# Performance work log

Hardware: AMD Instinct MI355X
Metric: run time of the kernel (lower is better)

The kernel has to match this reference:

```python
import jax, jax.numpy as jnp
import numpy as np

B, S, HID = 1, 2048, 4096
NH, NKV, HD = 32, 8, 128
GROUPS = NH // NKV
EPS = 1e-8
THETA = 10000.0
SCALE = HD ** -0.5
INIT = 0.02


def setup_inputs() -> dict:
    key = jax.random.key(0)
    ks = jax.random.split(key, 8)
    return {
        "hidden_states": jax.random.normal(ks[0], (B, S, HID), jnp.float32),
        "position_ids": jnp.arange(S, dtype=jnp.int32)[None, :],
        "wq": jax.random.normal(ks[1], (HID, NH * HD), jnp.float32) * INIT,
        "wk": jax.random.normal(ks[2], (HID, NKV * HD), jnp.float32) * INIT,
        "wv": jax.random.normal(ks[3], (HID, NKV * HD), jnp.float32) * INIT,
        "wo": jax.random.normal(ks[4], (NH * HD, HID), jnp.float32) * INIT,
        "memory": jax.random.normal(ks[5], (NKV, HD, HD), jnp.float32) * INIT,
        "norm_m": jax.random.uniform(ks[6], (NKV, HD, HD), jnp.float32) * 0.5 + 0.5,
        "beta": jnp.zeros((1,), jnp.float32),
    }


def _rotate_half(x):
    h = x.shape[-1] // 2
    return jnp.concatenate([-x[..., h:], x[..., :h]], axis=-1)


def _rope(position_ids):
    inv_freq = 1.0 / (THETA ** (jnp.arange(0, HD, 2, dtype=jnp.float32) / HD))  # [HD/2]
    freqs = position_ids.astype(jnp.float32)[:, :, None] * inv_freq[None, None, :]  # [B,S,HD/2]
    emb = jnp.concatenate([freqs, freqs], axis=-1)  # [B,S,HD]
    return jnp.cos(emb)[:, None], jnp.sin(emb)[:, None]  # [B,1,S,HD] each


def reference(hidden_states, position_ids, wq, wk, wv, wo, memory, norm_m, beta):
    # projections -> [B, heads, S, HD]
    q = (hidden_states @ wq).reshape(B, S, NH, HD).transpose(0, 2, 1, 3)
    k = (hidden_states @ wk).reshape(B, S, NKV, HD).transpose(0, 2, 1, 3)
    v = (hidden_states @ wv).reshape(B, S, NKV, HD).transpose(0, 2, 1, 3)

    # ---- retrieve from compressive memory (pre-RoPE Q, as in original) ----
    qf = jax.nn.elu(q) + 1.0
    qn = qf / (qf.sum(axis=-1, keepdims=True) + EPS)            # [B,NH,S,HD]
    mem_t = jnp.tile(memory[None], (1, GROUPS, 1, 1))            # torch .repeat == tile: head h -> memory[h % NKV]
    norm_t = jnp.tile(jnp.swapaxes(norm_m, -1, -2)[None], (1, GROUPS, 1, 1))
    mem_out = jnp.matmul(qn, mem_t) / (jnp.matmul(qn, norm_t) + EPS)  # [B,NH,S,HD]

    # ---- delta-rule memory update (no-grad side effect in torch) ----
    kf = jax.nn.elu(k) + 1.0
    kn = kf / (kf.sum(axis=-1, keepdims=True) + EPS)             # [B,NKV,S,HD]
    v_ret = jnp.matmul(kn, memory) / (jnp.matmul(kn, jnp.swapaxes(norm_m, -1, -2)) + EPS)
    delta = jnp.einsum('bhsd,bhse->hde', kn, v - v_ret)          # sum over batch
    updated_memory = memory + delta
    updated_norm = norm_m + kn.sum(axis=2, keepdims=True)[0]     # [NKV,1,HD] broadcast

    # ---- RoPE ----
    cos, sin = _rope(position_ids)
    q = q * cos + _rotate_half(q) * sin
    k = k * cos + _rotate_half(k) * sin

    # ---- causal attention with GQA (repeat_interleave for K/V) ----
    kr = jnp.repeat(k, GROUPS, axis=1)
    vr = jnp.repeat(v, GROUPS, axis=1)
    scores = jnp.einsum('bhqd,bhkd->bhqk', q, kr) * SCALE        # [B,NH,S,S]
    causal = jnp.tril(jnp.ones((S, S), dtype=bool))
    scores = jnp.where(causal, scores, jnp.finfo(scores.dtype).min)
    attn = jax.nn.softmax(scores, axis=-1)
    attn_out = jnp.einsum('bhqk,bhkd->bhqd', attn, vr)           # [B,NH,S,HD]

    # ---- sigmoid-gated combine + output projection ----
    gate = jax.nn.sigmoid(beta)                                   # [1]
    combined = gate * mem_out + (1.0 - gate) * attn_out
    out = combined.transpose(0, 2, 1, 3).reshape(B, S, NH * HD) @ wo
    return out, updated_memory, updated_norm
```

## Files before the change

### kernel.cpp

```cpp
#include <hip/hip_runtime.h>

#define S_LEN 2048
#define HID_DIM 4096
#define NH 32
#define NKV 8
#define HD 128
#define QKV_N 6144
#define SCALE_F 0.08838834764831845f

typedef unsigned short u16;
typedef __attribute__((ext_vector_type(8))) __bf16 bf16x8;
typedef __attribute__((ext_vector_type(4))) float f32x4;

__device__ __forceinline__ u16 f2bf(float f) {
  unsigned u = __float_as_uint(f);
  return (u16)((u + 0x7fffu + ((u >> 16) & 1u)) >> 16);
}
__device__ __forceinline__ float bf2f(u16 v) {
  return __uint_as_float((unsigned)v << 16);
}

__device__ __forceinline__ void gl_lds16(const u16* g, u16* l) {
  __builtin_amdgcn_global_load_lds(
      (const __attribute__((address_space(1))) unsigned int*)g,
      (__attribute__((address_space(3))) unsigned int*)l, 16, 0, 0);
}


__global__ void k_f32_to_bf16(const float* __restrict__ in, u16* __restrict__ out, long n4) {
  long i = (long)blockIdx.x * blockDim.x + threadIdx.x;
  if (i >= n4) return;
  float4 v = ((const float4*)in)[i];
  ushort4 o;
  o.x = f2bf(v.x); o.y = f2bf(v.y); o.z = f2bf(v.z); o.w = f2bf(v.w);
  ((ushort4*)out)[i] = o;
}

__global__ void k_tr64(const float* __restrict__ in, u16* __restrict__ out,
                       int ld_in, int ld_out, long in_bs, long out_bs) {
  __shared__ float tile[64][65];
  const float* A = in + (long)blockIdx.z * in_bs;
  u16* O = out + (long)blockIdx.z * out_bs;
  int r0 = blockIdx.y * 64, c0 = blockIdx.x * 64;
  int tx = threadIdx.x & 31, ty = threadIdx.x >> 5;
#pragma unroll
  for (int i = 0; i < 8; i++) {
    int r = ty + 8 * i;
    float2 v = *(const float2*)&A[(long)(r0 + r) * ld_in + c0 + 2 * tx];
    tile[r][2 * tx] = v.x;
    tile[r][2 * tx + 1] = v.y;
  }
  __syncthreads();
#pragma unroll
  for (int i = 0; i < 8; i++) {
    int c = ty + 8 * i;
    ushort2 o;
    o.x = f2bf(tile[2 * tx][c]);
    o.y = f2bf(tile[2 * tx + 1][c]);
    *(ushort2*)&O[(long)(c0 + c) * ld_out + r0 + 2 * tx] = o;
  }
}

__global__ void k_norm_to_bc(const float* __restrict__ norm, u16* __restrict__ bc) {
  int h = blockIdx.y;
  int i = blockIdx.x * 256 + threadIdx.x;
  bc[(long)h * 32768 + 16384 + i] = f2bf(norm[(long)h * 16384 + i]);
}


__global__ __launch_bounds__(512, 2) void k_gemm8(
    const u16* __restrict__ A, const u16* __restrict__ Bt, void* __restrict__ Cv,
    int kloop, int lda, int ldb, int ldc,
    long strideA, long strideB, long strideC, int bmodB, int obf) {
  __shared__ __align__(16) u16 lds[65536];
  const int bz = blockIdx.z;
  const u16* Ap = A + (long)bz * strideA;
  const u16* Bp = Bt + (long)(bz % bmodB) * strideB;
  const long coff = (long)bz * strideC;

  const int gx = gridDim.x, gy = gridDim.y;
  const int nwg = gx * gy;
  int id = blockIdx.y * gx + blockIdx.x;
  if (!(nwg & 7)) { int q = nwg >> 3; id = (id & 7) * q + (id >> 3); }
  const int m0 = (id % gy) * 256;
  const int n0 = (id / gy) * 256;

  const int tid = threadIdx.x, wid = tid >> 6, lane = tid & 63;
  const int l15 = lane & 15, lhi = lane >> 4;
  const int wm = wid >> 2, wn = wid & 3;

  const int srow = (wid << 3) + (lane >> 3);
  const int ssw = ((lane & 7) ^ (lane >> 3)) * 8;
  auto stA = [&](int d, int g, long kt) {
    gl_lds16(Ap + (long)(m0 + g * 64 + srow) * lda + kt + ssw,
             &lds[d * 32768 + (g * 64 + (wid << 3)) * 64]);
  };
  auto stB = [&](int d, int g, long kt) {
    gl_lds16(Bp + (long)(n0 + g * 64 + srow) * ldb + kt + ssw,
             &lds[d * 32768 + 16384 + (g * 64 + (wid << 3)) * 64]);
  };

  const int swb = l15 & 7;
  const int aBase = (wm * 128 + l15) * 64;
  const int bBase = 16384 + (wn * 64 + l15) * 64;
  const int ko0 = (lhi ^ swb) * 8;
  const int ko1 = ((4 + lhi) ^ swb) * 8;

  const int KT = kloop >> 6;
  const int NIT = KT >> 1;

  f32x4 acc[8][4];
#pragma unroll
  for (int i = 0; i < 8; i++)
#pragma unroll
    for (int j = 0; j < 4; j++) acc[i][j] = (f32x4){0.f, 0.f, 0.f, 0.f};

#pragma unroll
  for (int g = 0; g < 4; g++) stA(0, g, 0);
#pragma unroll
  for (int g = 0; g < 4; g++) stB(0, g, 0);
#pragma unroll
  for (int g = 0; g < 4; g++) stB(1, g, 64);
  asm volatile("s_waitcnt vmcnt(4)" ::: "memory");
  __builtin_amdgcn_s_barrier();
  asm volatile("" ::: "memory");

  for (int t = 0; t < NIT; ++t) {
    const long kA = (long)(2 * t + 1) * 64;
    const long kB0 = (long)(2 * t + 2) * 64;
    const long kB1 = (long)(2 * t + 3) * 64;
    const bool st0 = (2 * t + 2) < KT;
    const bool st1 = (2 * t + 3) < KT;
    const bool last = (t + 1 == NIT);

    {
      const u16* lb = &lds[0];
      bf16x8 Bf[4][2];
#pragma unroll
      for (int p = 0; p < 4; p++) {
        if (p == 0) {
#pragma unroll
          for (int ni = 0; ni < 4; ni++) {
            Bf[ni][0] = *(const bf16x8*)&lb[bBase + ni * 1024 + ko0];
            Bf[ni][1] = *(const bf16x8*)&lb[bBase + ni * 1024 + ko1];
          }
        }
        bf16x8 a0k0 = *(const bf16x8*)&lb[aBase + (2 * p) * 1024 + ko0];
        bf16x8 a0k1 = *(const bf16x8*)&lb[aBase + (2 * p) * 1024 + ko1];
        bf16x8 a1k0 = *(const bf16x8*)&lb[aBase + (2 * p + 1) * 1024 + ko0];
        bf16x8 a1k1 = *(const bf16x8*)&lb[aBase + (2 * p + 1) * 1024 + ko1];
        if (p == 0) { stA(1, 0, kA); stA(1, 1, kA); }
        else if (p == 1) { stA(1, 2, kA); stA(1, 3, kA); }
        else if (p == 2) { if (st0) { stB(0, 0, kB0); stB(0, 1, kB0); } }
        else { if (st0) { stB(0, 2, kB0); stB(0, 3, kB0); } }
        asm volatile("" ::: "memory");
        if (p == 3) {
          if (last) asm volatile("s_waitcnt vmcnt(0)" ::: "memory");
          else      asm volatile("s_waitcnt vmcnt(4)" ::: "memory");
        }
        __builtin_amdgcn_s_barrier();
        asm volatile("" ::: "memory");
        __builtin_amdgcn_s_setprio(1);
#pragma unroll
        for (int ni = 0; ni < 4; ni++) {
          acc[2 * p][ni] = __builtin_amdgcn_mfma_f32_16x16x32_bf16(a0k0, Bf[ni][0], acc[2 * p][ni], 0, 0, 0);
          acc[2 * p][ni] = __builtin_amdgcn_mfma_f32_16x16x32_bf16(a0k1, Bf[ni][1], acc[2 * p][ni], 0, 0, 0);
          acc[2 * p + 1][ni] = __builtin_amdgcn_mfma_f32_16x16x32_bf16(a1k0, Bf[ni][0], acc[2 * p + 1][ni], 0, 0, 0);
          acc[2 * p + 1][ni] = __builtin_amdgcn_mfma_f32_16x16x32_bf16(a1k1, Bf[ni][1], acc[2 * p + 1][ni], 0, 0, 0);
        }
        __builtin_amdgcn_s_setprio(0);
        asm volatile("" ::: "memory");
        __builtin_amdgcn_s_barrier();
        asm volatile("" ::: "memory");
      }
    }
    {
      const u16* lb = &lds[32768];
      bf16x8 Bf[4][2];
#pragma unroll
      for (int p = 0; p < 4; p++) {
        if (p == 0) {
#pragma unroll
          for (int ni = 0; ni < 4; ni++) {
            Bf[ni][0] = *(const bf16x8*)&lb[bBase + ni * 1024 + ko0];
            Bf[ni][1] = *(const bf16x8*)&lb[bBase + ni * 1024 + ko1];
          }
        }
        bf16x8 a0k0 = *(const bf16x8*)&lb[aBase + (2 * p) * 1024 + ko0];
        bf16x8 a0k1 = *(const bf16x8*)&lb[aBase + (2 * p) * 1024 + ko1];
        bf16x8 a1k0 = *(const bf16x8*)&lb[aBase + (2 * p + 1) * 1024 + ko0];
        bf16x8 a1k1 = *(const bf16x8*)&lb[aBase + (2 * p + 1) * 1024 + ko1];
        if (p == 0) { if (st0) { stA(0, 0, kB0); stA(0, 1, kB0); } }
        else if (p == 1) { if (st0) { stA(0, 2, kB0); stA(0, 3, kB0); } }
        else if (p == 2) { if (st1) { stB(1, 0, kB1); stB(1, 1, kB1); } }
        else { if (st1) { stB(1, 2, kB1); stB(1, 3, kB1); } }
        asm volatile("" ::: "memory");
        if (p == 3 && !last) asm volatile("s_waitcnt vmcnt(4)" ::: "memory");
        __builtin_amdgcn_s_barrier();
        asm volatile("" ::: "memory");
        __builtin_amdgcn_s_setprio(1);
#pragma unroll
        for (int ni = 0; ni < 4; ni++) {
          acc[2 * p][ni] = __builtin_amdgcn_mfma_f32_16x16x32_bf16(a0k0, Bf[ni][0], acc[2 * p][ni], 0, 0, 0);
          acc[2 * p][ni] = __builtin_amdgcn_mfma_f32_16x16x32_bf16(a0k1, Bf[ni][1], acc[2 * p][ni], 0, 0, 0);
          acc[2 * p + 1][ni] = __builtin_amdgcn_mfma_f32_16x16x32_bf16(a1k0, Bf[ni][0], acc[2 * p + 1][ni], 0, 0, 0);
          acc[2 * p + 1][ni] = __builtin_amdgcn_mfma_f32_16x16x32_bf16(a1k1, Bf[ni][1], acc[2 * p + 1][ni], 0, 0, 0);
        }
        __builtin_amdgcn_s_setprio(0);
        asm volatile("" ::: "memory");
        __builtin_amdgcn_s_barrier();
        asm volatile("" ::: "memory");
      }
    }
  }

#pragma unroll
  for (int mi = 0; mi < 8; mi++)
#pragma unroll
    for (int ni = 0; ni < 4; ni++)
#pragma unroll
      for (int j = 0; j < 4; j++) {
        long row = m0 + wm * 128 + mi * 16 + lhi * 4 + j;
        long col = n0 + wn * 64 + ni * 16 + l15;
        if (obf)
          ((u16*)Cv)[coff + row * ldc + col] = f2bf(acc[mi][ni][j]);
        else
          ((float*)Cv)[coff + row * ldc + col] = acc[mi][ni][j];
      }
}


__global__ void k_addp(const u16* __restrict__ p0, const u16* __restrict__ p1,
                       float* __restrict__ out) {
  long i = ((long)blockIdx.x * 256 + threadIdx.x) * 8;
  ushort4 a0 = *(const ushort4*)&p0[i], a1 = *(const ushort4*)&p0[i + 4];
  ushort4 b0 = *(const ushort4*)&p1[i], b1 = *(const ushort4*)&p1[i + 4];
  float4 o0, o1;
  o0.x = bf2f(a0.x) + bf2f(b0.x); o0.y = bf2f(a0.y) + bf2f(b0.y);
  o0.z = bf2f(a0.z) + bf2f(b0.z); o0.w = bf2f(a0.w) + bf2f(b0.w);
  o1.x = bf2f(a1.x) + bf2f(b1.x); o1.y = bf2f(a1.y) + bf2f(b1.y);
  o1.z = bf2f(a1.z) + bf2f(b1.z); o1.w = bf2f(a1.w) + bf2f(b1.w);
  *(float4*)&out[i] = o0;
  *(float4*)&out[i + 4] = o1;
}


__global__ void k_qnrope(const float* __restrict__ qkv, const int* __restrict__ pos,
                         u16* __restrict__ qnb, u16* __restrict__ qrb,
                         u16* __restrict__ knb, u16* __restrict__ krb,
                         float* __restrict__ knf) {
  int s = blockIdx.x, y = blockIdx.y, l = threadIdx.x;
  bool isq = y < NH;
  int h = isq ? y : y - NH;
  const float* row = qkv + (long)s * QKV_N + (isq ? h * HD : HID_DIM + h * HD);
  float x0 = row[l], x1 = row[l + 64];
  float f0 = x0 > 0.f ? x0 + 1.f : __expf(x0);
  float f1 = x1 > 0.f ? x1 + 1.f : __expf(x1);
  float sum = f0 + f1;
#pragma unroll
  for (int m = 32; m >= 1; m >>= 1) sum += __shfl_xor(sum, m);
  float inv = 1.f / (sum + 1e-8f);
  float y0 = f0 * inv, y1 = f1 * inv;
  long o = ((long)h * S_LEN + s) * HD;
  float p = (float)pos[s];
  float ang = p * expf(-(float)l * (9.210340371976184f / 64.0f));
  float c = cosf(ang), sn = sinf(ang);
  u16 r0 = f2bf(x0 * c - x1 * sn), r1 = f2bf(x1 * c + x0 * sn);
  if (isq) {
    qnb[o + l] = f2bf(y0); qnb[o + l + 64] = f2bf(y1);
    qrb[o + l] = r0; qrb[o + l + 64] = r1;
  } else {
    knb[o + l] = f2bf(y0); knb[o + l + 64] = f2bf(y1);
    knf[o + l] = y0; knf[o + l + 64] = y1;
    krb[o + l] = r0; krb[o + l + 64] = r1;
  }
}


__global__ void k_uvret(const u16* __restrict__ rawk, const float* __restrict__ qkv,
                        float* __restrict__ U) {
  int s = blockIdx.x, h = blockIdx.y, e = threadIdx.x;
  long base = ((long)h * S_LEN + s) * 256;
  float num = bf2f(rawk[base + e]), den = bf2f(rawk[base + 128 + e]);
  U[((long)h * S_LEN + s) * HD + e] =
      qkv[(long)s * QKV_N + HID_DIM + NKV * HD + h * HD + e] - num / (den + 1e-8f);
}


__global__ __launch_bounds__(256, 2) void k_flash3(
    const u16* __restrict__ qr, const u16* __restrict__ kr,
    const u16* __restrict__ vt, float* __restrict__ attn) {
  __shared__ u16 KV[2][16384];
  __shared__ u16 Ps[4][16 * 64];
  const int bx = blockIdx.x, h = blockIdx.y;
  const int hk = h >> 2;
  const int tid = threadIdx.x, wid = tid >> 6, lane = tid & 63;
  const int l15 = lane & 15, lhi = lane >> 4;
  const u16* qbase = qr + (long)h * S_LEN * HD;
  const u16* kb0 = kr + (long)hk * S_LEN * HD;
  const u16* vb0 = vt + (long)hk * HD * S_LEN;
  float* ob = attn + (long)h * S_LEN * HD;
  u16* P = Ps[wid];

  int kr_r[4], kr_sc[4], vr_r[4], vr_sc[4];
#pragma unroll
  for (int it = 0; it < 4; it++) {
    int chunk = it * 4 + wid;
    kr_r[it] = chunk * 4 + (lane >> 4);
    kr_sc[it] = ((lane & 15) * 8) ^ ((kr_r[it] & 7) * 8);
    vr_r[it] = chunk * 8 + (lane >> 3);
    vr_sc[it] = ((lane & 7) * 8) ^ ((vr_r[it] & 7) * 8);
  }

  for (int si = 0; si < 2; si++) {
    const int s = si ? (31 - bx) : bx;
    const int qs = s * 64 + wid * 16;
    bf16x8 aq[4];
#pragma unroll
    for (int kc = 0; kc < 4; kc++)
      aq[kc] = *(const bf16x8*)&qbase[(long)(qs + l15) * HD + kc * 32 + lhi * 8];
    f32x4 accO[8];
#pragma unroll
    for (int i = 0; i < 8; i++) accO[i] = (f32x4){0.f, 0.f, 0.f, 0.f};
    float rs[4] = {0.f, 0.f, 0.f, 0.f};

    if (si) __syncthreads();
    {
      u16* Kb = KV[0];
#pragma unroll
      for (int it = 0; it < 4; it++)
        gl_lds16(kb0 + (long)kr_r[it] * HD + kr_sc[it], &Kb[(it * 4 + wid) * 512]);
#pragma unroll
      for (int it = 0; it < 4; it++)
        gl_lds16(vb0 + (long)vr_r[it] * S_LEN + vr_sc[it], &Kb[8192 + (it * 4 + wid) * 512]);
    }
    int cur = 0;

    for (int t = 0; t <= s; t++) {
      asm volatile("s_waitcnt vmcnt(0)" ::: "memory");
      __syncthreads();
      if (t < s) {
        u16* Kb = KV[cur ^ 1];
        const long kt = (long)(t + 1) * 64;
#pragma unroll
        for (int it = 0; it < 4; it++)
          gl_lds16(kb0 + (kt + kr_r[it]) * HD + kr_sc[it], &Kb[(it * 4 + wid) * 512]);
#pragma unroll
        for (int it = 0; it < 4; it++)
          gl_lds16(vb0 + (long)vr_r[it] * S_LEN + kt + vr_sc[it], &Kb[8192 + (it * 4 + wid) * 512]);
      }
      const u16* Ks = KV[cur];
      const u16* Vs = Ks + 8192;

      f32x4 accS[4];
#pragma unroll
      for (int i = 0; i < 4; i++) accS[i] = (f32x4){0.f, 0.f, 0.f, 0.f};
#pragma unroll
      for (int ni = 0; ni < 4; ni++) {
        int row = ni * 16 + l15;
#pragma unroll
        for (int kc = 0; kc < 4; kc++) {
          bf16x8 bk = *(const bf16x8*)&Ks[row * 128 + ((kc * 32 + lhi * 8) ^ ((row & 7) * 8))];
          accS[ni] = __builtin_amdgcn_mfma_f32_16x16x32_bf16(aq[kc], bk, accS[ni], 0, 0, 0);
        }
      }
      const bool diag = (t == s);
#pragma unroll
      for (int ni = 0; ni < 4; ni++) {
        int col = t * 64 + ni * 16 + l15;
#pragma unroll
        for (int j = 0; j < 4; j++) {
          int row = qs + lhi * 4 + j;
          float p = (!diag || col <= row) ? __expf(accS[ni][j] * SCALE_F) : 0.f;
          rs[j] += p;
          int pr = lhi * 4 + j;
          P[pr * 64 + ((ni * 16 + l15) ^ ((pr & 7) * 8))] = f2bf(p);
        }
      }
      asm volatile("s_waitcnt lgkmcnt(0)" ::: "memory");
      __builtin_amdgcn_sched_barrier(0);
      bf16x8 ap[2];
#pragma unroll
      for (int ks = 0; ks < 2; ks++)
        ap[ks] = *(const bf16x8*)&P[l15 * 64 + ((ks * 32 + lhi * 8) ^ ((l15 & 7) * 8))];
#pragma unroll
      for (int nj = 0; nj < 8; nj++) {
        int row = nj * 16 + l15;
#pragma unroll
        for (int ks = 0; ks < 2; ks++) {
          bf16x8 bv = *(const bf16x8*)&Vs[row * 64 + ((ks * 32 + lhi * 8) ^ ((row & 7) * 8))];
          accO[nj] = __builtin_amdgcn_mfma_f32_16x16x32_bf16(ap[ks], bv, accO[nj], 0, 0, 0);
        }
      }
      cur ^= 1;
    }
#pragma unroll
    for (int j = 0; j < 4; j++) {
      float v = rs[j];
      v += __shfl_xor(v, 1);
      v += __shfl_xor(v, 2);
      v += __shfl_xor(v, 4);
      v += __shfl_xor(v, 8);
      rs[j] = 1.f / v;
    }
#pragma unroll
    for (int nj = 0; nj < 8; nj++)
#pragma unroll
      for (int j = 0; j < 4; j++)
        ob[(long)(qs + lhi * 4 + j) * HD + nj * 16 + l15] = accO[nj][j] * rs[j];
  }
}


__global__ void k_combine(const u16* __restrict__ rawq, const float* __restrict__ attn,
                          const float* __restrict__ beta, u16* __restrict__ comb) {
  int s = blockIdx.x, h = blockIdx.y, d = threadIdx.x;
  float g = 1.f / (1.f + __expf(-beta[0]));
  long b = ((long)h * S_LEN + s) * 256;
  float mo = bf2f(rawq[b + d]) / (bf2f(rawq[b + 128 + d]) + 1e-8f);
  float ao = attn[((long)h * S_LEN + s) * HD + d];
  comb[(long)s * HID_DIM + h * HD + d] = f2bf(g * mo + (1.f - g) * ao);
}


__global__ void k_delta_part(const float* __restrict__ knf, const float* __restrict__ U,
                             float* __restrict__ dpart) {
  int d0 = blockIdx.x * 16, h = blockIdx.y, c = blockIdx.z, e = threadIdx.x;
  const float* kh = knf + (long)h * S_LEN * HD + (long)c * 512 * HD;
  const float* Uh = U + (long)h * S_LEN * HD + (long)c * 512 * HD;
  float a[16];
#pragma unroll
  for (int d = 0; d < 16; d++) a[d] = 0.f;
  for (int s = 0; s < 512; s++) {
    float u = Uh[(long)s * HD + e];
    const float* kr = &kh[(long)s * HD + d0];
#pragma unroll
    for (int d = 0; d < 16; d++) a[d] += kr[d] * u;
  }
  long ob = (long)c * (NKV * HD * HD) + (long)h * HD * HD + (long)d0 * HD + e;
#pragma unroll
  for (int d = 0; d < 16; d++) dpart[ob + (long)d * HD] = a[d];
}

__global__ void k_delta_reduce(const float* __restrict__ dpart, const float* __restrict__ mem,
                               float* __restrict__ outmem) {
  long i = (long)blockIdx.x * 256 + threadIdx.x;
  const long N = (long)NKV * HD * HD;
  float a = dpart[i] + dpart[N + i] + dpart[2 * N + i] + dpart[3 * N + i];
  outmem[i] = mem[i] + a;
}

__global__ void k_norm_part(const float* __restrict__ knf, float* __restrict__ npart) {
  int c = blockIdx.x, h = blockIdx.y, j = threadIdx.x;
  const float* kh = knf + (long)h * S_LEN * HD + (long)c * 128 * HD;
  float a = 0.f;
  for (int s = 0; s < 128; s++) a += kh[(long)s * HD + j];
  npart[((long)c * NKV + h) * HD + j] = a;
}

__global__ void k_norm_write(const float* __restrict__ npart, const float* __restrict__ norm,
                             float* __restrict__ outn) {
  int h = blockIdx.x, j = threadIdx.x & 127;
  int r = blockIdx.y * 2 + (threadIdx.x >> 7);
  float cs = 0.f;
#pragma unroll
  for (int c = 0; c < 16; c++) cs += npart[((long)c * NKV + h) * HD + j];
  long o = (long)h * HD * HD + (long)r * HD + j;
  outn[o] = norm[o] + cs;
}


extern "C" void kernel_launch(void* const* d_in, const int* in_sizes, int n_in,
                              void* d_out, int out_size, void* d_ws, size_t ws_size,
                              hipStream_t stream) {
  const float* hs = (const float*)d_in[0];
  const int* pos = (const int*)d_in[1];
  const float* wq = (const float*)d_in[2];
  const float* wk = (const float*)d_in[3];
  const float* wv = (const float*)d_in[4];
  const float* wo = (const float*)d_in[5];
  const float* memf = (const float*)d_in[6];
  const float* normf = (const float*)d_in[7];
  const float* beta = (const float*)d_in[8];
  (void)in_sizes; (void)n_in; (void)out_size; (void)ws_size;

  float* out = (float*)d_out;
  float* out_mem = out + (long)S_LEN * HID_DIM;
  float* out_norm = out_mem + NKV * HD * HD;

  const size_t MB = 1u << 20;
  char* w = (char*)d_ws;
  u16* hsb    = (u16*)(w + 0);
  u16* qnb    = (u16*)(w + 0);
  u16* comb   = (u16*)(w + 0);
  float* dpart= (float*)(w + 0);
  float* npart= (float*)(w + 2 * MB);
  u16* wT6    = (u16*)(w + 16 * MB);
  u16* rawq   = (u16*)(w + 16 * MB);
  u16* woT    = (u16*)(w + 16 * MB);
  u16* rawk   = (u16*)(w + 48 * MB);
  u16* bc     = (u16*)(w + 57 * MB);
  u16* vtb    = (u16*)(w + 57 * MB + 512 * 1024);
  float* qkvf = (float*)(w + 66 * MB + 512 * 1024);
  float* attn = (float*)(w + 66 * MB + 512 * 1024);
  u16* p0     = (u16*)(w + 98 * MB + 512 * 1024);
  float* Ub   = (float*)(w + 114 * MB + 512 * 1024);
  float* knf  = (float*)(w + 122 * MB + 512 * 1024);
  u16* qrb    = (u16*)(w + 130 * MB + 512 * 1024);
  u16* p1     = (u16*)(w + 130 * MB + 512 * 1024);
  u16* krb    = (u16*)(w + 146 * MB + 512 * 1024);
  u16* knb    = (u16*)(w + 150 * MB + 512 * 1024);

  k_f32_to_bf16<<<dim3((S_LEN * HID_DIM / 4 + 255) / 256), dim3(256), 0, stream>>>(
      hs, hsb, (long)(S_LEN * HID_DIM / 4));
  k_tr64<<<dim3(64, 64, 1), dim3(256), 0, stream>>>(
      wq, wT6, HID_DIM, HID_DIM, 0L, 0L);
  k_tr64<<<dim3(16, 64, 1), dim3(256), 0, stream>>>(
      wk, wT6 + (long)HID_DIM * HID_DIM, 1024, HID_DIM, 0L, 0L);
  k_tr64<<<dim3(16, 64, 1), dim3(256), 0, stream>>>(
      wv, wT6 + (long)(HID_DIM + 1024) * HID_DIM, 1024, HID_DIM, 0L, 0L);
  k_gemm8<<<dim3(QKV_N / 256, S_LEN / 256, 1), dim3(512), 0, stream>>>(
      hsb, wT6, qkvf, HID_DIM, HID_DIM, HID_DIM, QKV_N, 0L, 0L, 0L, 1, 0);

  k_qnrope<<<dim3(S_LEN, NH + NKV), dim3(64), 0, stream>>>(
      qkvf, pos, qnb, qrb, knb, krb, knf);

  k_tr64<<<dim3(2, 32, NKV), dim3(256), 0, stream>>>(
      qkvf + HID_DIM + NKV * HD, vtb, QKV_N, S_LEN, 128L, (long)(HD * S_LEN));
  k_tr64<<<dim3(2, 2, NKV), dim3(256), 0, stream>>>(
      memf, bc, HD, HD, (long)(HD * HD), (long)(256 * HD));
  k_norm_to_bc<<<dim3(64, NKV), dim3(256), 0, stream>>>(normf, bc);

  k_gemm8<<<dim3(1, 8, NH), dim3(512), 0, stream>>>(
      qnb, bc, rawq, HD, HD, HD, 256, (long)(S_LEN * HD), (long)(256 * HD),
      (long)(S_LEN * 256), NKV, 1);
  k_gemm8<<<dim3(1, 8, NKV), dim3(512), 0, stream>>>(
      knb, bc, rawk, HD, HD, HD, 256, (long)(S_LEN * HD), (long)(256 * HD),
      (long)(S_LEN * 256), NKV, 1);

  k_uvret<<<dim3(S_LEN, NKV), dim3(128), 0, stream>>>(rawk, qkvf, Ub);

  k_flash3<<<dim3(16, NH), dim3(256), 0, stream>>>(qrb, krb, vtb, attn);

  k_combine<<<dim3(S_LEN, NH), dim3(128), 0, stream>>>(rawq, attn, beta, comb);

  k_tr64<<<dim3(64, 64, 1), dim3(256), 0, stream>>>(
      wo, woT, HID_DIM, HID_DIM, 0L, 0L);
  k_gemm8<<<dim3(HID_DIM / 256, S_LEN / 256, 2), dim3(512), 0, stream>>>(
      comb, woT, p0, 2048, HID_DIM, HID_DIM, HID_DIM,
      2048L, 2048L, (long)(p1 - p0), 2, 1);
  k_addp<<<dim3(S_LEN * HID_DIM / 2048), dim3(256), 0, stream>>>(p0, p1, out);

  k_delta_part<<<dim3(8, NKV, 4), dim3(128), 0, stream>>>(knf, Ub, dpart);
  k_delta_reduce<<<dim3(512), dim3(256), 0, stream>>>(dpart, memf, out_mem);
  k_norm_part<<<dim3(16, NKV), dim3(128), 0, stream>>>(knf, npart);
  k_norm_write<<<dim3(NKV, 64), dim3(256), 0, stream>>>(npart, normf, out_norm);
}
```

Baseline: 435.1 us.

## Fuse gated combine into flash epilogue and fold small memory-path kernels

The gated combine now happens in the flash-attention epilogue, which writes bf16 `comb` directly instead of a full fp32 attention buffer that a separate pass reread. The v - v_ret computation moves from its own kernel into the delta accumulation. The Q and K memory-retrieval GEMMs run as one batched launch through a new second A pointer. The fp32 copy of normalized K is dropped and the delta and norm reductions read the bf16 values. The aim is to cut memory traffic and launch count, at the cost of slightly lower precision in the memory-update outputs and extra rawq reads inside the attention kernel's epilogue.

```diff
diff --git a/kernel.cpp b/kernel.cpp
--- a/kernel.cpp
+++ b/kernel.cpp
@@ -69,12 +69,14 @@
 
 
 __global__ __launch_bounds__(512, 2) void k_gemm8(
-    const u16* __restrict__ A, const u16* __restrict__ Bt, void* __restrict__ Cv,
+    const u16* __restrict__ A, const u16* __restrict__ A2, int zsplit,
+    const u16* __restrict__ Bt, void* __restrict__ Cv,
     int kloop, int lda, int ldb, int ldc,
     long strideA, long strideB, long strideC, int bmodB, int obf) {
   __shared__ __align__(16) u16 lds[65536];
   const int bz = blockIdx.z;
-  const u16* Ap = A + (long)bz * strideA;
+  const u16* Ap = (bz < zsplit) ? (A + (long)bz * strideA)
+                                : (A2 + (long)(bz - zsplit) * strideA);
   const u16* Bp = Bt + (long)(bz % bmodB) * strideB;
   const long coff = (long)bz * strideC;
 
@@ -247,8 +249,7 @@
 
 __global__ void k_qnrope(const float* __restrict__ qkv, const int* __restrict__ pos,
                          u16* __restrict__ qnb, u16* __restrict__ qrb,
-                         u16* __restrict__ knb, u16* __restrict__ krb,
-                         float* __restrict__ knf) {
+                         u16* __restrict__ knb, u16* __restrict__ krb) {
   int s = blockIdx.x, y = blockIdx.y, l = threadIdx.x;
   bool isq = y < NH;
   int h = isq ? y : y - NH;
@@ -271,25 +272,15 @@
     qrb[o + l] = r0; qrb[o + l + 64] = r1;
   } else {
     knb[o + l] = f2bf(y0); knb[o + l + 64] = f2bf(y1);
-    knf[o + l] = y0; knf[o + l + 64] = y1;
     krb[o + l] = r0; krb[o + l + 64] = r1;
   }
 }
 
 
-__global__ void k_uvret(const u16* __restrict__ rawk, const float* __restrict__ qkv,
-                        float* __restrict__ U) {
-  int s = blockIdx.x, h = blockIdx.y, e = threadIdx.x;
-  long base = ((long)h * S_LEN + s) * 256;
-  float num = bf2f(rawk[base + e]), den = bf2f(rawk[base + 128 + e]);
-  U[((long)h * S_LEN + s) * HD + e] =
-      qkv[(long)s * QKV_N + HID_DIM + NKV * HD + h * HD + e] - num / (den + 1e-8f);
-}
-
-
-__global__ __launch_bounds__(256, 2) void k_flash3(
+__global__ __launch_bounds__(256, 2) void k_flash4(
     const u16* __restrict__ qr, const u16* __restrict__ kr,
-    const u16* __restrict__ vt, float* __restrict__ attn) {
+    const u16* __restrict__ vt, const u16* __restrict__ rawq,
+    const float* __restrict__ beta, u16* __restrict__ comb) {
   __shared__ u16 KV[2][16384];
   __shared__ u16 Ps[4][16 * 64];
   const int bx = blockIdx.x, h = blockIdx.y;
@@ -299,8 +290,8 @@
   const u16* qbase = qr + (long)h * S_LEN * HD;
   const u16* kb0 = kr + (long)hk * S_LEN * HD;
   const u16* vb0 = vt + (long)hk * HD * S_LEN;
-  float* ob = attn + (long)h * S_LEN * HD;
   u16* P = Ps[wid];
+  const float g = 1.f / (1.f + __expf(-beta[0]));
 
   int kr_r[4], kr_sc[4], vr_r[4], vr_sc[4];
 #pragma unroll
@@ -406,36 +397,34 @@
 #pragma unroll
     for (int nj = 0; nj < 8; nj++)
 #pragma unroll
-      for (int j = 0; j < 4; j++)
-        ob[(long)(qs + lhi * 4 + j) * HD + nj * 16 + l15] = accO[nj][j] * rs[j];
-  }
-}
-
-
-__global__ void k_combine(const u16* __restrict__ rawq, const float* __restrict__ attn,
-                          const float* __restrict__ beta, u16* __restrict__ comb) {
-  int s = blockIdx.x, h = blockIdx.y, d = threadIdx.x;
-  float g = 1.f / (1.f + __expf(-beta[0]));
-  long b = ((long)h * S_LEN + s) * 256;
-  float mo = bf2f(rawq[b + d]) / (bf2f(rawq[b + 128 + d]) + 1e-8f);
-  float ao = attn[((long)h * S_LEN + s) * HD + d];
-  comb[(long)s * HID_DIM + h * HD + d] = f2bf(g * mo + (1.f - g) * ao);
-}
-
-
-__global__ void k_delta_part(const float* __restrict__ knf, const float* __restrict__ U,
-                             float* __restrict__ dpart) {
+      for (int j = 0; j < 4; j++) {
+        int row = qs + lhi * 4 + j;
+        int col = nj * 16 + l15;
+        long rb = ((long)h * S_LEN + row) * 256 + col;
+        float mo = bf2f(rawq[rb]) / (bf2f(rawq[rb + 128]) + 1e-8f);
+        float ao = accO[nj][j] * rs[j];
+        comb[(long)row * HID_DIM + h * HD + col] = f2bf(g * mo + (1.f - g) * ao);
+      }
+  }
+}
+
+
+__global__ void k_delta_part(const u16* __restrict__ knb, const u16* __restrict__ rawk,
+                             const float* __restrict__ qkv, float* __restrict__ dpart) {
   int d0 = blockIdx.x * 16, h = blockIdx.y, c = blockIdx.z, e = threadIdx.x;
-  const float* kh = knf + (long)h * S_LEN * HD + (long)c * 512 * HD;
-  const float* Uh = U + (long)h * S_LEN * HD + (long)c * 512 * HD;
+  const u16* kh = knb + (long)h * S_LEN * HD + (long)c * 512 * HD;
+  const u16* rk = rawk + ((long)h * S_LEN + (long)c * 512) * 256;
+  const float* vb = qkv + HID_DIM + NKV * HD + h * HD + (long)c * 512 * QKV_N;
   float a[16];
 #pragma unroll
   for (int d = 0; d < 16; d++) a[d] = 0.f;
   for (int s = 0; s < 512; s++) {
-    float u = Uh[(long)s * HD + e];
-    const float* kr = &kh[(long)s * HD + d0];
-#pragma unroll
-    for (int d = 0; d < 16; d++) a[d] += kr[d] * u;
+    float num = bf2f(rk[(long)s * 256 + e]);
+    float den = bf2f(rk[(long)s * 256 + 128 + e]);
+    float u = vb[(long)s * QKV_N + e] - num / (den + 1e-8f);
+    const u16* kr = &kh[(long)s * HD + d0];
+#pragma unroll
+    for (int d = 0; d < 16; d++) a[d] += bf2f(kr[d]) * u;
   }
   long ob = (long)c * (NKV * HD * HD) + (long)h * HD * HD + (long)d0 * HD + e;
 #pragma unroll
@@ -450,11 +439,11 @@
   outmem[i] = mem[i] + a;
 }
 
-__global__ void k_norm_part(const float* __restrict__ knf, float* __restrict__ npart) {
+__global__ void k_norm_part(const u16* __restrict__ knb, float* __restrict__ npart) {
   int c = blockIdx.x, h = blockIdx.y, j = threadIdx.x;
-  const float* kh = knf + (long)h * S_LEN * HD + (long)c * 128 * HD;
+  const u16* kh = knb + (long)h * S_LEN * HD + (long)c * 128 * HD;
   float a = 0.f;
-  for (int s = 0; s < 128; s++) a += kh[(long)s * HD + j];
+  for (int s = 0; s < 128; s++) a += bf2f(kh[(long)s * HD + j]);
   npart[((long)c * NKV + h) * HD + j] = a;
 }
 
@@ -493,8 +482,6 @@
   u16* hsb    = (u16*)(w + 0);
   u16* qnb    = (u16*)(w + 0);
   u16* comb   = (u16*)(w + 0);
-  float* dpart= (float*)(w + 0);
-  float* npart= (float*)(w + 2 * MB);
   u16* wT6    = (u16*)(w + 16 * MB);
   u16* rawq   = (u16*)(w + 16 * MB);
   u16* woT    = (u16*)(w + 16 * MB);
@@ -502,13 +489,12 @@
   u16* bc     = (u16*)(w + 57 * MB);
   u16* vtb    = (u16*)(w + 57 * MB + 512 * 1024);
   float* qkvf = (float*)(w + 66 * MB + 512 * 1024);
-  float* attn = (float*)(w + 66 * MB + 512 * 1024);
   u16* p0     = (u16*)(w + 98 * MB + 512 * 1024);
-  float* Ub   = (float*)(w + 114 * MB + 512 * 1024);
-  float* knf  = (float*)(w + 122 * MB + 512 * 1024);
   u16* qrb    = (u16*)(w + 130 * MB + 512 * 1024);
   u16* p1     = (u16*)(w + 130 * MB + 512 * 1024);
   u16* krb    = (u16*)(w + 146 * MB + 512 * 1024);
+  float* dpart= (float*)(w + 146 * MB + 512 * 1024);
+  float* npart= (float*)(w + 148 * MB + 512 * 1024);
   u16* knb    = (u16*)(w + 150 * MB + 512 * 1024);
 
   k_f32_to_bf16<<<dim3((S_LEN * HID_DIM / 4 + 255) / 256), dim3(256), 0, stream>>>(
@@ -520,10 +506,11 @@
   k_tr64<<<dim3(16, 64, 1), dim3(256), 0, stream>>>(
       wv, wT6 + (long)(HID_DIM + 1024) * HID_DIM, 1024, HID_DIM, 0L, 0L);
   k_gemm8<<<dim3(QKV_N / 256, S_LEN / 256, 1), dim3(512), 0, stream>>>(
-      hsb, wT6, qkvf, HID_DIM, HID_DIM, HID_DIM, QKV_N, 0L, 0L, 0L, 1, 0);
+      hsb, hsb, 1 << 30, wT6, qkvf, HID_DIM, HID_DIM, HID_DIM, QKV_N,
+      0L, 0L, 0L, 1, 0);
 
   k_qnrope<<<dim3(S_LEN, NH + NKV), dim3(64), 0, stream>>>(
-      qkvf, pos, qnb, qrb, knb, krb, knf);
+      qkvf, pos, qnb, qrb, knb, krb);
 
   k_tr64<<<dim3(2, 32, NKV), dim3(256), 0, stream>>>(
       qkvf + HID_DIM + NKV * HD, vtb, QKV_N, S_LEN, 128L, (long)(HD * S_LEN));
@@ -531,28 +518,21 @@
       memf, bc, HD, HD, (long)(HD * HD), (long)(256 * HD));
   k_norm_to_bc<<<dim3(64, NKV), dim3(256), 0, stream>>>(normf, bc);
 
-  k_gemm8<<<dim3(1, 8, NH), dim3(512), 0, stream>>>(
-      qnb, bc, rawq, HD, HD, HD, 256, (long)(S_LEN * HD), (long)(256 * HD),
-      (long)(S_LEN * 256), NKV, 1);
-  k_gemm8<<<dim3(1, 8, NKV), dim3(512), 0, stream>>>(
-      knb, bc, rawk, HD, HD, HD, 256, (long)(S_LEN * HD), (long)(256 * HD),
-      (long)(S_LEN * 256), NKV, 1);
-
-  k_uvret<<<dim3(S_LEN, NKV), dim3(128), 0, stream>>>(rawk, qkvf, Ub);
-
-  k_flash3<<<dim3(16, NH), dim3(256), 0, stream>>>(qrb, krb, vtb, attn);
-
-  k_combine<<<dim3(S_LEN, NH), dim3(128), 0, stream>>>(rawq, attn, beta, comb);
+  k_gemm8<<<dim3(1, 8, NH + NKV), dim3(512), 0, stream>>>(
+      qnb, knb, NH, bc, rawq, HD, HD, HD, 256,
+      (long)(S_LEN * HD), (long)(256 * HD), (long)(S_LEN * 256), NKV, 1);
+
+  k_flash4<<<dim3(16, NH), dim3(256), 0, stream>>>(qrb, krb, vtb, rawq, beta, comb);
+
+  k_delta_part<<<dim3(8, NKV, 4), dim3(128), 0, stream>>>(knb, rawk, qkvf, dpart);
+  k_delta_reduce<<<dim3(512), dim3(256), 0, stream>>>(dpart, memf, out_mem);
+  k_norm_part<<<dim3(16, NKV), dim3(128), 0, stream>>>(knb, npart);
+  k_norm_write<<<dim3(NKV, 64), dim3(256), 0, stream>>>(npart, normf, out_norm);
 
   k_tr64<<<dim3(64, 64, 1), dim3(256), 0, stream>>>(
       wo, woT, HID_DIM, HID_DIM, 0L, 0L);
   k_gemm8<<<dim3(HID_DIM / 256, S_LEN / 256, 2), dim3(512), 0, stream>>>(
-      comb, woT, p0, 2048, HID_DIM, HID_DIM, HID_DIM,
+      comb, comb, 1 << 30, woT, p0, 2048, HID_DIM, HID_DIM, HID_DIM,
       2048L, 2048L, (long)(p1 - p0), 2, 1);
   k_addp<<<dim3(S_LEN * HID_DIM / 2048), dim3(256), 0, stream>>>(p0, p1, out);
-
-  k_delta_part<<<dim3(8, NKV, 4), dim3(128), 0, stream>>>(knf, Ub, dpart);
-  k_delta_reduce<<<dim3(512), dim3(256), 0, stream>>>(dpart, memf, out_mem);
-  k_norm_part<<<dim3(16, NKV), dim3(128), 0, stream>>>(knf, npart);
-  k_norm_write<<<dim3(NKV, 64), dim3(256), 0, stream>>>(npart, normf, out_norm);
-}
+}
```

Result: slower. 550.1 us (+26.4%).
